# Optimization experiments

Hardware: AMD Instinct MI355X
Metric: run time of the kernel (lower is better)

Reference implementation:

```python
import jax, jax.numpy as jnp
import numpy as np
from jax import lax

D_MODEL = 1024
D_STATE = 16
D_CONV = 4
EXPAND = 2
HEADDIM = 64
D_INNER = EXPAND * D_MODEL            # 2048
NHEADS = D_INNER // HEADDIM           # 32
NGROUPS = 1
CONV_DIM = D_INNER + 2 * NGROUPS * D_STATE   # 2080
D_IN_PROJ = 2 * D_INNER + 2 * NGROUPS * D_STATE + NHEADS  # 4160
EPS = 1e-5


def _mamba2(x, in_proj_w, conv_w, conv_b, dt_bias, A_log, Dp, norm_w, out_proj_w):
    # x: (B, L, D_MODEL)
    Bt, L, _ = x.shape
    zxbcdt = jnp.einsum('bld,ed->ble', x, in_proj_w)  # (B,L,D_IN_PROJ)
    z, xBC, dt = jnp.split(zxbcdt, [D_INNER, D_INNER + CONV_DIM], axis=-1)
    dt = jax.nn.softplus(dt + dt_bias)               # (B,L,H)
    # depthwise causal conv over time
    xBC = jnp.swapaxes(xBC, 1, 2)                    # (B,C,L)
    xBC = lax.conv_general_dilated(
        xBC, conv_w, window_strides=(1,), padding=[(D_CONV - 1, 0)],
        feature_group_count=CONV_DIM,
        dimension_numbers=('NCH', 'OIH', 'NCH')) + conv_b[None, :, None]
    xBC = jnp.swapaxes(jax.nn.silu(xBC), 1, 2)       # (B,L,C)
    xs, Bm, Cm = jnp.split(xBC, [D_INNER, D_INNER + D_STATE], axis=-1)
    xs = xs.reshape(Bt, L, NHEADS, HEADDIM)          # (B,L,H,P)
    A = -jnp.exp(A_log)                              # (H,)
    dA = jnp.exp(dt * A)                             # (B,L,H)

    def step(h, inp):
        dA_t, dt_t, B_t, C_t, x_t = inp              # (B,H),(B,H),(B,N),(B,N),(B,H,P)
        h = h * dA_t[:, :, None, None] + jnp.einsum('bh,bn,bhp->bhpn', dt_t, B_t, x_t)
        y = jnp.einsum('bn,bhpn->bhp', C_t, h)
        return h, y

    h0 = jnp.zeros((Bt, NHEADS, HEADDIM, D_STATE), x.dtype)
    xs_seq = (jnp.swapaxes(dA, 0, 1), jnp.swapaxes(dt, 0, 1),
              jnp.swapaxes(Bm, 0, 1), jnp.swapaxes(Cm, 0, 1),
              jnp.swapaxes(xs, 0, 1))
    _, ys = lax.scan(step, h0, xs_seq)               # ys: (L,B,H,P)
    y = jnp.swapaxes(ys, 0, 1) + Dp[None, None, :, None] * xs
    y = y.reshape(Bt, L, D_INNER)
    # gated RMSNorm: gate first (norm_before_gate=False), then rmsnorm
    y = y * jax.nn.silu(z)
    y = y * lax.rsqrt(jnp.mean(y * y, axis=-1, keepdims=True) + EPS) * norm_w
    return jnp.einsum('bld,od->blo', y, out_proj_w)  # (B,L,D_MODEL)


def setup_inputs() -> dict:
    key = jax.random.key(0)
    ks = jax.random.split(key, 20)
    B, L = 2, 2048
    def mamba_params(kidx):
        k = jax.random.split(ks[kidx], 8)
        return dict(
            in_proj_w=jax.random.normal(k[0], (D_IN_PROJ, D_MODEL), jnp.float32) / np.sqrt(D_MODEL),
            conv_w=jax.random.normal(k[1], (CONV_DIM, 1, D_CONV), jnp.float32) / np.sqrt(D_CONV),
            conv_b=jax.random.normal(k[2], (CONV_DIM,), jnp.float32) * 0.01,
            dt_bias=jnp.log(jnp.expm1(jax.random.uniform(k[3], (NHEADS,), jnp.float32, 1e-3, 0.1))),
            A_log=jnp.log(jax.random.uniform(k[4], (NHEADS,), jnp.float32, 1.0, 16.0)),
            Dp=jnp.ones((NHEADS,), jnp.float32),
            norm_w=jnp.ones((D_INNER,), jnp.float32),
            out_proj_w=jax.random.normal(k[5], (D_MODEL, D_INNER), jnp.float32) / np.sqrt(D_INNER),
        )
    pf = mamba_params(1)
    pb = mamba_params(2)
    inp = {'x': jax.random.normal(ks[0], (B, L, D_MODEL), jnp.float32)}
    for name, p in (('fwd', pf), ('bwd', pb)):
        for pk, pv in p.items():
            inp[f'{name}_{pk}'] = pv
    inp['layer_out_proj_w'] = jax.random.normal(ks[3], (D_MODEL, 2 * D_MODEL), jnp.float32) / np.sqrt(2 * D_MODEL)
    inp['layer_scale'] = jnp.full((D_MODEL,), 1e-4, jnp.float32)
    return inp


def reference(x,
              fwd_in_proj_w, fwd_conv_w, fwd_conv_b, fwd_dt_bias, fwd_A_log, fwd_Dp, fwd_norm_w, fwd_out_proj_w,
              bwd_in_proj_w, bwd_conv_w, bwd_conv_b, bwd_dt_bias, bwd_A_log, bwd_Dp, bwd_norm_w, bwd_out_proj_w,
              layer_out_proj_w, layer_scale):
    h_fwd = _mamba2(x, fwd_in_proj_w, fwd_conv_w, fwd_conv_b, fwd_dt_bias, fwd_A_log, fwd_Dp, fwd_norm_w, fwd_out_proj_w)
    x_rev = jnp.flip(x, axis=1)
    h_bwd = jnp.flip(_mamba2(x_rev, bwd_in_proj_w, bwd_conv_w, bwd_conv_b, bwd_dt_bias, bwd_A_log, bwd_Dp, bwd_norm_w, bwd_out_proj_w), axis=1)
    h_bi = jnp.concatenate([h_fwd, h_bwd], axis=-1)   # (B,L,2*D_MODEL)
    mamba_out = jnp.einsum('ble,de->bld', h_bi, layer_out_proj_w)
    # dropout is identity in eval mode
    return x + mamba_out * layer_scale
```

## Files before the change

### kernel.cpp

```cpp
#include <hip/hip_runtime.h>

typedef __attribute__((ext_vector_type(8))) short bf16x8;
typedef __attribute__((ext_vector_type(4))) float f32x4;
typedef __attribute__((ext_vector_type(2))) long i64x2;

#define DEV static __device__ __forceinline__

DEV float b2f(unsigned short u) {
    union { unsigned int u; float f; } c; c.u = ((unsigned int)u) << 16; return c.f;
}
DEV unsigned short f2b(float f) {
    union { float f; unsigned int u; } c; c.f = f;
    unsigned int u = c.u + 0x7fffu + ((c.u >> 16) & 1u);
    return (unsigned short)(u >> 16);
}
DEV float silu_f(float v) { return v / (1.f + __expf(-v)); }

DEV unsigned short cvtpk2(float a, float b) {
    unsigned int d;
    asm("v_cvt_pk_fp8_f32 %0, %1, %2" : "=v"(d) : "v"(a), "v"(b));
    return (unsigned short)d;
}
DEV unsigned char cvt1(float a) { return (unsigned char)cvtpk2(a, 0.f); }

DEV int kperm(int gc) {
    return (gc & ~63) | (((gc >> 3) & 3) << 4) | (((gc >> 5) & 1) << 3) | (gc & 7);
}

#define GLD16(gp, lp) __builtin_amdgcn_global_load_lds( \
    (const __attribute__((address_space(1))) void*)(gp), \
    (__attribute__((address_space(3))) void*)(lp), 16, 0, 0)

#define LSEQ 2048
#define NB 2
#define RTOT 4096
#define DM 1024
#define DI 2048
#define NH 32
#define HP 64
#define NSTATE 16
#define CDIM 2080
#define DIP 4160
#define NW 8320
#define NWP 8448
#define QCH 64
#define NCH (LSEQ / QCH)

struct Cvt8Jobs {
    const float* s0[4];
    const float* s1[4];
    unsigned char* dst[4];
    int rows0[4], rows1[4], rowstot[4], shift[4];
};
__global__ __launch_bounds__(256) void cvt8b_kernel(Cvt8Jobs j) {
    const int jb = blockIdx.y;
    const int gid = blockIdx.x * 256 + threadIdx.x;
    const int shift = j.shift[jb];
    const int tpr = 1 << shift;
    if (gid >= (j.rowstot[jb] << shift)) return;
    const int row = gid >> shift, g = gid & (tpr - 1);
    const int blk = g >> 3, sub = g & 7, lq = sub >> 1, ks = sub & 1;
    const int K = tpr << 3;
    uint2 o;
    const int r0 = j.rows0[jb], r1 = j.rows1[jb];
    if (row < r0 + r1) {
        const float* src = (row < r0 ? j.s0[jb] + (size_t)row * K
                                     : j.s1[jb] + (size_t)(row - r0) * K)
                           + blk * 64 + ks * 32 + lq * 8;
        float4 v0 = *(const float4*)src;
        float4 v1 = *(const float4*)(src + 4);
        o.x = (unsigned)cvtpk2(v0.x, v0.y) | ((unsigned)cvtpk2(v0.z, v0.w) << 16);
        o.y = (unsigned)cvtpk2(v1.x, v1.y) | ((unsigned)cvtpk2(v1.z, v1.w) << 16);
    } else {
        o.x = 0; o.y = 0;
    }
    *(uint2*)(j.dst[jb] + (size_t)row * K + blk * 64 + sub * 8) = o;
}

template<int BM, int BN, int EPI>
__global__ void __launch_bounds__(512, 4)
gemm8_kernel(
    const unsigned char* __restrict__ A0, const unsigned char* __restrict__ B0,
    const unsigned char* __restrict__ A1, const unsigned char* __restrict__ B1,
    void* __restrict__ Cout,
    int Ntot, int K, int ldc, int coff0, int coff1,
    const float* __restrict__ ex, const float* __restrict__ esc)
{
    constexpr int NT = 512;
    constexpr int MF = BM / 32;
    constexpr int NI = BN / 64;
    constexpr int ABYTES = BM * 64;
    constexpr int BBYTES = BN * 64;
    constexpr int BUFB = ABYTES + BBYTES;
    constexpr int QA = ABYTES / (NT * 16);
    constexpr int QB = BBYTES / (NT * 16);
    constexpr int GT = QA + QB;
    __shared__ unsigned char lds8[4 * BUFB];

    const unsigned char* __restrict__ A8 = blockIdx.z ? A1 : A0;
    const unsigned char* __restrict__ B8 = blockIdx.z ? B1 : B0;
    const int coff = blockIdx.z ? coff1 : coff0;

    const int nbx = gridDim.x, nby = gridDim.y;
    const int nwg = nbx * nby;
    int id = blockIdx.y * nbx + blockIdx.x;
    {
        const int q = nwg >> 3, r = nwg & 7;
        const int xcd = id & 7, off = id >> 3;
        id = (xcd < r) ? (xcd * (q + 1) + off) : (r * (q + 1) + (xcd - r) * q + off);
    }
    const int gm = 8;
    const int gidx = id / (gm * nbx);
    const int rem  = id - gidx * gm * nbx;
    const int width = min(gm, nby - gidx * gm);
    const int bm = (gidx * gm + rem % width) * BM;
    const int bn = (rem / width) * BN;

    const int tid  = threadIdx.x;
    const int wave = tid >> 6, lane = tid & 63;
    const int wm = wave >> 2, wn = wave & 3;
    const int lr = lane & 15, lq = lane >> 4;
    const int KT = K >> 6;

    int aoff[MF], boff[NI];
#pragma unroll
    for (int mf = 0; mf < MF; ++mf) {
        int row = wm * (BM / 2) + mf * 16 + lr;
        int L = row >> 1, cc = ((row & 1) << 2) | lq;
        aoff[mf] = L * 128 + ((cc ^ (L & 7)) << 4);
    }
#pragma unroll
    for (int ni = 0; ni < NI; ++ni) {
        int row = wn * (BN / 4) + ni * 16 + lr;
        int L = row >> 1, cc = ((row & 1) << 2) | lq;
        boff[ni] = ABYTES + L * 128 + ((cc ^ (L & 7)) << 4);
    }

    auto stage = [&](int ktt, int sbuf) {
#pragma unroll
        for (int q = 0; q < QA; ++q) {
            int u = q * NT + tid;
            int L = u >> 3, cp = u & 7;
            int cc = cp ^ (L & 7);
            int srow = bm + 2 * L + (cc >> 2);
            const unsigned char* src = A8 + (size_t)srow * K + (ktt << 6) + ((cc & 3) << 4);
            GLD16(src, &lds8[sbuf * BUFB + q * (NT * 16) + (wave << 10)]);
        }
#pragma unroll
        for (int q = 0; q < QB; ++q) {
            int u = q * NT + tid;
            int L = u >> 3, cp = u & 7;
            int cc = cp ^ (L & 7);
            int srow = bn + 2 * L + (cc >> 2);
            const unsigned char* src = B8 + (size_t)srow * K + (ktt << 6) + ((cc & 3) << 4);
            GLD16(src, &lds8[sbuf * BUFB + ABYTES + q * (NT * 16) + (wave << 10)]);
        }
    };

    f32x4 acc[MF][NI];
#pragma unroll
    for (int i = 0; i < MF; ++i)
#pragma unroll
        for (int j = 0; j < NI; ++j) acc[i][j] = (f32x4){0.f, 0.f, 0.f, 0.f};

    stage(0, 0);
    if (KT > 1) stage(1, 1);
    if (KT > 2) stage(2, 2);
    if (KT > 2)      { asm volatile("s_waitcnt vmcnt(%0)" :: "n"(2 * GT) : "memory"); }
    else if (KT > 1) { asm volatile("s_waitcnt vmcnt(%0)" :: "n"(GT) : "memory"); }
    else             { asm volatile("s_waitcnt vmcnt(0)" ::: "memory"); }
    __builtin_amdgcn_sched_barrier(0);
    __builtin_amdgcn_s_barrier();
    __builtin_amdgcn_sched_barrier(0);

    for (int kt = 0; kt < KT; ++kt) {
        const int cb = (kt & 3) * BUFB;
        if (kt + 3 < KT) stage(kt + 3, (kt + 3) & 3);

        i64x2 av[MF], bv[NI];
#pragma unroll
        for (int mf = 0; mf < MF; ++mf) av[mf] = *(const i64x2*)&lds8[cb + aoff[mf]];
#pragma unroll
        for (int ni = 0; ni < NI; ++ni) bv[ni] = *(const i64x2*)&lds8[cb + boff[ni]];

        __builtin_amdgcn_s_setprio(1);
#pragma unroll
        for (int mf = 0; mf < MF; ++mf)
#pragma unroll
            for (int ni = 0; ni < NI; ++ni) {
                acc[mf][ni] = __builtin_amdgcn_mfma_f32_16x16x32_fp8_fp8(av[mf].x, bv[ni].x, acc[mf][ni], 0, 0, 0);
                acc[mf][ni] = __builtin_amdgcn_mfma_f32_16x16x32_fp8_fp8(av[mf].y, bv[ni].y, acc[mf][ni], 0, 0, 0);
            }
        __builtin_amdgcn_s_setprio(0);

        if (kt + 1 < KT) {
            if (kt + 3 < KT)      { asm volatile("s_waitcnt vmcnt(%0)" :: "n"(2 * GT) : "memory"); }
            else if (kt + 2 < KT) { asm volatile("s_waitcnt vmcnt(%0)" :: "n"(GT) : "memory"); }
            else                  { asm volatile("s_waitcnt vmcnt(0)" ::: "memory"); }
            __builtin_amdgcn_sched_barrier(0);
            __builtin_amdgcn_s_barrier();
            __builtin_amdgcn_sched_barrier(0);
        }
    }

#pragma unroll
    for (int mf = 0; mf < MF; ++mf)
#pragma unroll
        for (int ni = 0; ni < NI; ++ni)
#pragma unroll
            for (int r = 0; r < 4; ++r) {
                int grow = bm + wm * (BM / 2) + mf * 16 + lq * 4 + r;
                int gcol = bn + wn * (BN / 4) + ni * 16 + lr;
                float v = acc[mf][ni][r];
                if (EPI == 1) {
                    if (gcol < Ntot)
                        ((unsigned short*)Cout)[(size_t)grow * ldc + coff + gcol] = f2b(v);
                } else if (EPI == 2) {
                    size_t idx = (size_t)grow * ldc + gcol;
                    ((float*)Cout)[idx] = ex[idx] + v * esc[gcol];
                } else {
                    int gc = coff + gcol;
                    ((unsigned char*)Cout)[(size_t)grow * ldc + kperm(gc)] = cvt1(v);
                }
            }
}

#define TCV 32
__global__ __launch_bounds__(256) void conv_kernel(
    const unsigned short* __restrict__ ZX,
    const float* __restrict__ cwF, const float* __restrict__ cbF,
    const float* __restrict__ cwB, const float* __restrict__ cbB,
    const float* __restrict__ dtbiasF, const float* __restrict__ AlogF,
    const float* __restrict__ dtbiasB, const float* __restrict__ AlogB,
    unsigned short* __restrict__ xs,
    float* __restrict__ Bc, float* __restrict__ Cc,
    float* __restrict__ dtb, float* __restrict__ dAb)
{
    const int c = blockIdx.x * 256 + threadIdx.x;
    const int t0 = blockIdx.y * TCV;
    const int db = blockIdx.z;
    const int d = db >> 1, b = db & 1;

    if (c >= CDIM) {
        if (c >= CDIM + NH) return;
        const int h = c - CDIM;
        const float bias = (d ? dtbiasB : dtbiasF)[h];
        const float A = -__expf((d ? AlogB : AlogF)[h]);
        const unsigned short* zp = ZX + (size_t)d * DIP + (DI + CDIM) + h;
#pragma unroll 4
        for (int i = 0; i < TCV; ++i) {
            int t = t0 + i;
            float raw = b2f(zp[((size_t)b * LSEQ + t) * NW]);
            float xv = raw + bias;
            float dtv = (xv > 20.f) ? xv : __logf(1.f + __expf(xv));
            int idx = (db * LSEQ + t) * NH + h;
            dtb[idx] = dtv;
            dAb[idx] = __expf(dtv * A);
        }
        return;
    }

    const float* cw = d ? cwB : cwF;
    const float* cb = d ? cbB : cbF;
    float4 w = *(const float4*)&cw[c * 4];
    const float bias = cb[c];
    const unsigned short* base = ZX + (size_t)d * DIP + DI + c;

    auto ldg = [&](int t) -> float {
        return (t >= 0 && t < LSEQ) ? b2f(base[(size_t)(b * LSEQ + t) * NW]) : 0.f;
    };
    auto emit = [&](int t, float acc) {
        float v = silu_f(acc);
        const int row = b * LSEQ + t;
        if (c < DI) {
            xs[((size_t)d * RTOT + row) * DI + c] = f2b(v);
        } else if (c < DI + NSTATE) {
            Bc[((size_t)db * LSEQ + t) * NSTATE + (c - DI)] = v;
        } else {
            Cc[((size_t)db * LSEQ + t) * NSTATE + (c - DI - NSTATE)] = v;
        }
    };

    if (d == 0) {
        float v0 = ldg(t0 - 3), v1 = ldg(t0 - 2), v2 = ldg(t0 - 1), vt = ldg(t0);
#pragma unroll 4
        for (int i = 0; i < TCV; ++i) {
            float vn = (i < TCV - 1) ? ldg(t0 + i + 1) : 0.f;
            emit(t0 + i, bias + w.x * v0 + w.y * v1 + w.z * v2 + w.w * vt);
            v0 = v1; v1 = v2; v2 = vt; vt = vn;
        }
    } else {
        float v3 = ldg(t0 + TCV + 2), v2 = ldg(t0 + TCV + 1), v1 = ldg(t0 + TCV), vt = ldg(t0 + TCV - 1);
#pragma unroll 4
        for (int i = TCV - 1; i >= 0; --i) {
            float vn = (i > 0) ? ldg(t0 + i - 1) : 0.f;
            emit(t0 + i, bias + w.w * vt + w.z * v1 + w.y * v2 + w.x * v3);
            v3 = v2; v2 = v1; v1 = vt; vt = vn;
        }
    }
}

#define LD16V(dst, ptr) do { const float4* _p = (const float4*)(ptr); \
    float4 _q0 = _p[0], _q1 = _p[1], _q2 = _p[2], _q3 = _p[3]; \
    dst[0]=_q0.x; dst[1]=_q0.y; dst[2]=_q0.z; dst[3]=_q0.w; \
    dst[4]=_q1.x; dst[5]=_q1.y; dst[6]=_q1.z; dst[7]=_q1.w; \
    dst[8]=_q2.x; dst[9]=_q2.y; dst[10]=_q2.z; dst[11]=_q2.w; \
    dst[12]=_q3.x; dst[13]=_q3.y; dst[14]=_q3.z; dst[15]=_q3.w; } while (0)

#define ST16V(ptr, src) do { float4* _p = (float4*)(ptr); \
    _p[0] = make_float4(src[0],src[1],src[2],src[3]); \
    _p[1] = make_float4(src[4],src[5],src[6],src[7]); \
    _p[2] = make_float4(src[8],src[9],src[10],src[11]); \
    _p[3] = make_float4(src[12],src[13],src[14],src[15]); } while (0)

__global__ __launch_bounds__(64) void chunk_state_kernel(
    const unsigned short* __restrict__ xs,
    const float* __restrict__ Bc,
    const float* __restrict__ dtb, const float* __restrict__ dAb,
    float* __restrict__ Sbuf,
    float* __restrict__ Pbuf)
{
    const int h = blockIdx.x, db = blockIdx.y, c = blockIdx.z;
    const int d = db >> 1, b = db & 1;
    const int lane = threadIdx.x;
    float hs[16];
#pragma unroll
    for (int n = 0; n < 16; ++n) hs[n] = 0.f;
    float pacc = 1.f;
    const size_t dbase = (size_t)d * RTOT;
    const int s0 = c * QCH;

    float xq0, xq1, xq2, xq3, dtq0, dtq1, dtq2, dtq3, dAq0, dAq1, dAq2, dAq3;
    float BA[16], BB[16];

#define SIDX(ii) (d ? (LSEQ - 1 - (s0 + min((ii), QCH - 1))) : (s0 + min((ii), QCH - 1)))
#define XL(S, ii) do { const int _t = SIDX(ii); \
    const size_t _row = (size_t)b * LSEQ + _t, _rdb = (size_t)db * LSEQ + _t; \
    xq##S = b2f(xs[(dbase + _row) * DI + h * HP + lane]); \
    dtq##S = dtb[_rdb * 32 + h]; dAq##S = dAb[_rdb * 32 + h]; } while (0)
#define BL(BUF, ii) do { const int _t = SIDX(ii); \
    const size_t _rdb = (size_t)db * LSEQ + _t; LD16V(BUF, Bc + _rdb * 16); } while (0)
#define SC(S, BUF) do { const float _dtx = dtq##S * xq##S; \
    _Pragma("unroll") for (int n = 0; n < 16; ++n) hs[n] = fmaf(hs[n], dAq##S, BUF[n] * _dtx); \
    pacc *= dAq##S; } while (0)

    XL(0, 0); XL(1, 1); XL(2, 2);
    BL(BA, 0);
    for (int ii = 0; ii < QCH; ii += 4) {
        XL(3, ii + 3); BL(BB, ii + 1); SC(0, BA);
        XL(0, ii + 4); BL(BA, ii + 2); SC(1, BB);
        XL(1, ii + 5); BL(BB, ii + 3); SC(2, BA);
        XL(2, ii + 6); BL(BA, ii + 4); SC(3, BB);
    }
#undef SIDX
#undef XL
#undef BL
#undef SC

    float* Sp = Sbuf + (((size_t)(db * NH + h)) * NCH + c) * 1024 + lane * 16;
    ST16V(Sp, hs);
    if (lane == 0) Pbuf[(db * NH + h) * NCH + c] = pacc;
}

__global__ __launch_bounds__(64) void chunk_combine_kernel(
    const float* __restrict__ Sbuf, const float* __restrict__ Pbuf,
    float* __restrict__ Hbuf)
{
    const int idx = blockIdx.x;
    const int lane = threadIdx.x;
    float hs[16];
#pragma unroll
    for (int n = 0; n < 16; ++n) hs[n] = 0.f;
    float* H0 = Hbuf + ((size_t)idx * NCH) * 1024 + lane * 16;
    ST16V(H0, hs);
    for (int c = 0; c < NCH - 1; ++c) {
        const float* Sp = Sbuf + ((size_t)idx * NCH + c) * 1024 + lane * 16;
        float S[16];
        LD16V(S, Sp);
        const float P = Pbuf[idx * NCH + c];
#pragma unroll
        for (int n = 0; n < 16; ++n) hs[n] = fmaf(hs[n], P, S[n]);
        float* Hp = Hbuf + ((size_t)idx * NCH + c + 1) * 1024 + lane * 16;
        ST16V(Hp, hs);
    }
}

__global__ __launch_bounds__(64) void chunk_scan_kernel(
    const unsigned short* __restrict__ xs,
    const float* __restrict__ Bc, const float* __restrict__ Cc,
    const float* __restrict__ dtb, const float* __restrict__ dAb,
    const float* __restrict__ DpF, const float* __restrict__ DpB,
    const float* __restrict__ Hbuf,
    unsigned short* __restrict__ ybuf)
{
    const int h = blockIdx.x, db = blockIdx.y, c = blockIdx.z;
    const int d = db >> 1, b = db & 1;
    const int lane = threadIdx.x;
    const float Dp = (d ? DpB : DpF)[h];
    float hs[16];
    {
        const float* Hp = Hbuf + ((size_t)(db * NH + h) * NCH + c) * 1024 + lane * 16;
        LD16V(hs, Hp);
    }
    const size_t dbase = (size_t)d * RTOT;
    const int s0 = c * QCH;

    float xq0, xq1, xq2, xq3, dtq0, dtq1, dtq2, dtq3, dAq0, dAq1, dAq2, dAq3;
    float BA[16], BB[16], CA[16], CB[16];

#define SIDX(ii) (d ? (LSEQ - 1 - (s0 + min((ii), QCH - 1))) : (s0 + min((ii), QCH - 1)))
#define XL(S, ii) do { const int _t = SIDX(ii); \
    const size_t _row = (size_t)b * LSEQ + _t, _rdb = (size_t)db * LSEQ + _t; \
    xq##S = b2f(xs[(dbase + _row) * DI + h * HP + lane]); \
    dtq##S = dtb[_rdb * 32 + h]; dAq##S = dAb[_rdb * 32 + h]; } while (0)
#define BLC(BUF, CBUF, ii) do { const int _t = SIDX(ii); \
    const size_t _rdb = (size_t)db * LSEQ + _t; \
    LD16V(BUF, Bc + _rdb * 16); LD16V(CBUF, Cc + _rdb * 16); } while (0)
#define SCY(S, BUF, CBUF, iv) do { const float _dtx = dtq##S * xq##S; \
    float _y0 = 0.f, _y1 = 0.f, _y2 = 0.f, _y3 = 0.f; \
    _Pragma("unroll") for (int n = 0; n < 16; n += 4) { \
        hs[n]   = fmaf(hs[n],   dAq##S, BUF[n]   * _dtx); _y0 = fmaf(CBUF[n],   hs[n],   _y0); \
        hs[n+1] = fmaf(hs[n+1], dAq##S, BUF[n+1] * _dtx); _y1 = fmaf(CBUF[n+1], hs[n+1], _y1); \
        hs[n+2] = fmaf(hs[n+2], dAq##S, BUF[n+2] * _dtx); _y2 = fmaf(CBUF[n+2], hs[n+2], _y2); \
        hs[n+3] = fmaf(hs[n+3], dAq##S, BUF[n+3] * _dtx); _y3 = fmaf(CBUF[n+3], hs[n+3], _y3); } \
    const int _t = d ? (LSEQ - 1 - (s0 + (iv))) : (s0 + (iv)); \
    const size_t _row = (size_t)b * LSEQ + _t; \
    ybuf[(dbase + _row) * DI + h * HP + lane] = f2b(((_y0 + _y1) + (_y2 + _y3)) + Dp * xq##S); } while (0)

    XL(0, 0); XL(1, 1); XL(2, 2);
    BLC(BA, CA, 0);
    for (int ii = 0; ii < QCH; ii += 4) {
        XL(3, ii + 3); BLC(BB, CB, ii + 1); SCY(0, BA, CA, ii);
        XL(0, ii + 4); BLC(BA, CA, ii + 2); SCY(1, BB, CB, ii + 1);
        XL(1, ii + 5); BLC(BB, CB, ii + 3); SCY(2, BA, CA, ii + 2);
        XL(2, ii + 6); BLC(BA, CA, ii + 4); SCY(3, BB, CB, ii + 3);
    }
#undef SIDX
#undef XL
#undef BLC
#undef SCY
}

__global__ __launch_bounds__(256) void gatenorm_kernel(
    const unsigned short* __restrict__ ybuf, const unsigned short* __restrict__ ZX,
    const float* __restrict__ nwF, const float* __restrict__ nwB,
    unsigned char* __restrict__ yg8)
{
    const int r = blockIdx.x;
    const int d = blockIdx.y;
    const int tid = threadIdx.x;
    const float* nw = d ? nwB : nwF;
    const int c0 = tid * 8;
    const unsigned short* yp = ybuf + ((size_t)d * RTOT + r) * DI + c0;
    const unsigned short* zp = ZX + (size_t)r * NW + d * DIP + c0;
    uint4 yv = *(const uint4*)yp;
    uint4 zv = *(const uint4*)zp;
    unsigned int yw[4] = {yv.x, yv.y, yv.z, yv.w};
    unsigned int zw[4] = {zv.x, zv.y, zv.z, zv.w};
    float g[8]; float ss = 0.f;
#pragma unroll
    for (int i = 0; i < 8; ++i) {
        unsigned short yu = (i & 1) ? (unsigned short)(yw[i >> 1] >> 16) : (unsigned short)(yw[i >> 1] & 0xffff);
        unsigned short zu = (i & 1) ? (unsigned short)(zw[i >> 1] >> 16) : (unsigned short)(zw[i >> 1] & 0xffff);
        float y = b2f(yu), z = b2f(zu);
        float gv = y * silu_f(z);
        g[i] = gv; ss += gv * gv;
    }
#pragma unroll
    for (int m = 1; m < 64; m <<= 1) ss += __shfl_xor(ss, m, 64);
    __shared__ float red[4];
    if ((tid & 63) == 0) red[tid >> 6] = ss;
    __syncthreads();
    float tot = red[0] + red[1] + red[2] + red[3];
    float sc = rsqrtf(tot * (1.f / 2048.f) + 1e-5f);
    uint2 o;
    o.x = (unsigned)cvtpk2(g[0] * sc * nw[c0 + 0], g[1] * sc * nw[c0 + 1])
        | ((unsigned)cvtpk2(g[2] * sc * nw[c0 + 2], g[3] * sc * nw[c0 + 3]) << 16);
    o.y = (unsigned)cvtpk2(g[4] * sc * nw[c0 + 4], g[5] * sc * nw[c0 + 5])
        | ((unsigned)cvtpk2(g[6] * sc * nw[c0 + 6], g[7] * sc * nw[c0 + 7]) << 16);
    const int pos = (c0 & ~63) | (((c0 >> 3) & 3) << 4) | (((c0 >> 5) & 1) << 3);
    *(uint2*)(yg8 + ((size_t)d * RTOT + r) * DI + pos) = o;
}

extern "C" void kernel_launch(void* const* d_in, const int* in_sizes, int n_in,
                              void* d_out, int out_size, void* d_ws, size_t ws_size,
                              hipStream_t stream)
{
    const float* x     = (const float*)d_in[0];
    const float* fin   = (const float*)d_in[1];
    const float* fcw   = (const float*)d_in[2];
    const float* fcb   = (const float*)d_in[3];
    const float* fdtb  = (const float*)d_in[4];
    const float* fAlog = (const float*)d_in[5];
    const float* fDp   = (const float*)d_in[6];
    const float* fnw   = (const float*)d_in[7];
    const float* fout  = (const float*)d_in[8];
    const float* bin   = (const float*)d_in[9];
    const float* bcw   = (const float*)d_in[10];
    const float* bcb   = (const float*)d_in[11];
    const float* bdtb  = (const float*)d_in[12];
    const float* bAlog = (const float*)d_in[13];
    const float* bDp   = (const float*)d_in[14];
    const float* bnw   = (const float*)d_in[15];
    const float* bout  = (const float*)d_in[16];
    const float* lw    = (const float*)d_in[17];
    const float* lsc   = (const float*)d_in[18];

    char* w = (char*)d_ws;
    auto alloc = [&](size_t bytes) { char* p = w; w += (bytes + 255) & ~(size_t)255; return p; };
    unsigned char*  xb8  = (unsigned char*)alloc((size_t)RTOT * DM);
    unsigned char*  win8 = (unsigned char*)alloc((size_t)NWP * DM);
    unsigned char*  wo8  = (unsigned char*)alloc((size_t)2 * DM * DI);
    unsigned char*  wl8  = (unsigned char*)alloc((size_t)DM * DI);
    unsigned short* zx  = (unsigned short*)alloc((size_t)RTOT * NW * 2);
    unsigned short* xs  = (unsigned short*)alloc((size_t)2 * RTOT * DI * 2);
    float* Bc  = (float*)alloc((size_t)2 * RTOT * NSTATE * 4);
    float* Cc  = (float*)alloc((size_t)2 * RTOT * NSTATE * 4);
    float* dtb = (float*)alloc((size_t)2 * RTOT * NH * 4);
    float* dAb = (float*)alloc((size_t)2 * RTOT * NH * 4);
    unsigned short* yb  = (unsigned short*)alloc((size_t)2 * RTOT * DI * 2);
    unsigned char*  yg8 = (unsigned char*)alloc((size_t)2 * RTOT * DI);
    unsigned char*  hbi8= (unsigned char*)alloc((size_t)RTOT * DI);
    float* Pbuf = (float*)alloc((size_t)128 * NCH * 4);
    float* Sbuf = (float*)alloc((size_t)128 * NCH * 1024 * 4);
    float* Hbuf = (float*)alloc((size_t)128 * NCH * 1024 * 4);
    (void)ws_size; (void)in_sizes; (void)n_in; (void)out_size;

    Cvt8Jobs j;
    j.s0[0] = x;    j.s1[0] = x;    j.dst[0] = xb8;  j.rows0[0] = RTOT; j.rows1[0] = 0;    j.rowstot[0] = RTOT; j.shift[0] = 7;
    j.s0[1] = fin;  j.s1[1] = bin;  j.dst[1] = win8; j.rows0[1] = DIP;  j.rows1[1] = DIP;  j.rowstot[1] = NWP;  j.shift[1] = 7;
    j.s0[2] = fout; j.s1[2] = bout; j.dst[2] = wo8;  j.rows0[2] = DM;   j.rows1[2] = DM;   j.rowstot[2] = 2 * DM; j.shift[2] = 8;
    j.s0[3] = lw;   j.s1[3] = lw;   j.dst[3] = wl8;  j.rows0[3] = DM;   j.rows1[3] = 0;    j.rowstot[3] = DM;   j.shift[3] = 8;
    cvt8b_kernel<<<dim3((NWP * 128 + 255) / 256, 4), 256, 0, stream>>>(j);

    gemm8_kernel<128, 128, 1><<<dim3(NWP / 128, RTOT / 128), 512, 0, stream>>>(
        xb8, win8, nullptr, nullptr, zx, NW, DM, NW, 0, 0, nullptr, nullptr);

    conv_kernel<<<dim3((CDIM + NH + 255) / 256, LSEQ / TCV, 4), 256, 0, stream>>>(
        zx, fcw, fcb, bcw, bcb, fdtb, fAlog, bdtb, bAlog, xs, Bc, Cc, dtb, dAb);

    chunk_state_kernel<<<dim3(NH, 4, NCH - 1), 64, 0, stream>>>(
        xs, Bc, dtb, dAb, Sbuf, Pbuf);
    chunk_combine_kernel<<<128, 64, 0, stream>>>(Sbuf, Pbuf, Hbuf);
    chunk_scan_kernel<<<dim3(NH, 4, NCH), 64, 0, stream>>>(
        xs, Bc, Cc, dtb, dAb, fDp, bDp, Hbuf, yb);

    gatenorm_kernel<<<dim3(RTOT, 2), 256, 0, stream>>>(yb, zx, fnw, bnw, yg8);

    gemm8_kernel<128, 128, 3><<<dim3(DM / 128, RTOT / 128, 2), 512, 0, stream>>>(
        yg8, wo8, yg8 + (size_t)RTOT * DI, wo8 + (size_t)DM * DI,
        hbi8, DM, DI, DI, 0, DM, nullptr, nullptr);

    gemm8_kernel<128, 128, 2><<<dim3(DM / 128, RTOT / 128), 512, 0, stream>>>(
        hbi8, wl8, nullptr, nullptr, d_out, DM, DI, DM, 0, 0, x, lsc);
}
```

Baseline: 296.5 us.

## Add 256x256 FP8 in-projection GEMM with triple-buffered ping-pong pipeline

Replaces the 128x128 FP8 GEMM used for the input projection with a new 256x256-tile kernel. The new kernel uses a three-stage LDS ring with async global-to-LDS loads, XCD-aware block remapping with grouped tile ordering, and interleaves LDS reads, next-stage loads and MFMA quarters between barriers with raised wave priority. It aims for more data reuse per tile and better overlap of memory with compute. The cost is one workgroup per CU with 96KB LDS, fewer blocks in flight, and tile-divisibility assumptions on M and padded N.

Measured after the change: 319.6 us. +7.8%, slower.

```diff
diff --git a/kernel.cpp b/kernel.cpp
--- a/kernel.cpp
+++ b/kernel.cpp
@@ -77,6 +77,158 @@
     *(uint2*)(j.dst[jb] + (size_t)row * K + blk * 64 + sub * 8) = o;
 }
 
+#define PBARWAIT \
+    __builtin_amdgcn_s_barrier(); __builtin_amdgcn_sched_barrier(0); \
+    asm volatile("s_waitcnt lgkmcnt(0)" ::: "memory"); \
+    __builtin_amdgcn_sched_barrier(0);
+#define PENDBAR \
+    __builtin_amdgcn_s_barrier(); __builtin_amdgcn_sched_barrier(0);
+
+#define PLDA(AV, base0, MH) \
+    AV[0] = *(const i64x2*)&lds8[(base0) + aoff[(MH)*4 + 0]]; \
+    AV[1] = *(const i64x2*)&lds8[(base0) + aoff[(MH)*4 + 1]]; \
+    AV[2] = *(const i64x2*)&lds8[(base0) + aoff[(MH)*4 + 2]]; \
+    AV[3] = *(const i64x2*)&lds8[(base0) + aoff[(MH)*4 + 3]];
+#define PLDB(baseB, J0) \
+    bv[0] = *(const i64x2*)&lds8[(baseB) + boff[(J0)]]; \
+    bv[1] = *(const i64x2*)&lds8[(baseB) + boff[(J0) + 1]];
+#define PMM(AV, MH, NH) \
+    __builtin_amdgcn_s_setprio(1); \
+    _Pragma("unroll") \
+    for (int i = 0; i < 4; ++i) \
+    _Pragma("unroll") \
+        for (int jj = 0; jj < 2; ++jj) { \
+            acc[(MH)*4 + i][(NH)*2 + jj] = __builtin_amdgcn_mfma_f32_16x16x32_fp8_fp8(AV[i].x, bv[jj].x, acc[(MH)*4 + i][(NH)*2 + jj], 0, 0, 0); \
+            acc[(MH)*4 + i][(NH)*2 + jj] = __builtin_amdgcn_mfma_f32_16x16x32_fp8_fp8(AV[i].y, bv[jj].y, acc[(MH)*4 + i][(NH)*2 + jj], 0, 0, 0); \
+        } \
+    __builtin_amdgcn_s_setprio(0);
+
+__global__ void __launch_bounds__(512, 1)
+gemm8p_kernel(const unsigned char* __restrict__ A8, const unsigned char* __restrict__ B8,
+              unsigned short* __restrict__ Cout, int Ntot, int K, int ldc)
+{
+    __shared__ unsigned char lds8[98304];
+
+    const int nbx = gridDim.x, nby = gridDim.y;
+    const int nwg = nbx * nby;
+    int id = blockIdx.y * nbx + blockIdx.x;
+    {
+        const int q = nwg >> 3, r = nwg & 7;
+        const int xcd = id & 7, off = id >> 3;
+        id = (xcd < r) ? (xcd * (q + 1) + off) : (r * (q + 1) + (xcd - r) * q + off);
+    }
+    const int gm = 8;
+    const int gidx = id / (gm * nbx);
+    const int rem  = id - gidx * gm * nbx;
+    const int width = min(gm, nby - gidx * gm);
+    const int bm = (gidx * gm + rem % width) * 256;
+    const int bn = (rem / width) * 256;
+
+    const int tid  = threadIdx.x;
+    const int wave = tid >> 6, lane = tid & 63;
+    const int wm = wave >> 2, wn = wave & 3;
+    const int lr = lane & 15, lq = lane >> 4;
+    const int KT = K >> 6;
+
+    int aoff[8], boff[4];
+#pragma unroll
+    for (int mf = 0; mf < 8; ++mf) {
+        int row = wm * 128 + mf * 16 + lr;
+        int L = row >> 1, cc = ((row & 1) << 2) | lq;
+        aoff[mf] = L * 128 + ((cc ^ (L & 7)) << 4);
+    }
+#pragma unroll
+    for (int ni = 0; ni < 4; ++ni) {
+        int row = wn * 64 + ni * 16 + lr;
+        int L = row >> 1, cc = ((row & 1) << 2) | lq;
+        boff[ni] = L * 128 + ((cc ^ (L & 7)) << 4);
+    }
+
+    auto stgA = [&](int ktt, int q, int buf) {
+        int u = q * 512 + tid;
+        int L = u >> 3, cp = u & 7;
+        int cc = cp ^ (L & 7);
+        int srow = bm + 2 * L + (cc >> 2);
+        const unsigned char* src = A8 + (size_t)srow * K + (ktt << 6) + ((cc & 3) << 4);
+        GLD16(src, &lds8[buf * 16384 + q * 8192 + (wave << 10)]);
+    };
+    auto stgB = [&](int ktt, int q, int buf) {
+        int u = q * 512 + tid;
+        int L = u >> 3, cp = u & 7;
+        int cc = cp ^ (L & 7);
+        int srow = bn + 2 * L + (cc >> 2);
+        const unsigned char* src = B8 + (size_t)srow * K + (ktt << 6) + ((cc & 3) << 4);
+        GLD16(src, &lds8[49152 + buf * 16384 + q * 8192 + (wave << 10)]);
+    };
+
+    f32x4 acc[8][4];
+#pragma unroll
+    for (int i = 0; i < 8; ++i)
+#pragma unroll
+        for (int j = 0; j < 4; ++j) acc[i][j] = (f32x4){0.f, 0.f, 0.f, 0.f};
+
+    stgA(0, 0, 0); stgA(0, 1, 0); stgB(0, 0, 0); stgB(0, 1, 0);
+    if (KT > 1) { stgA(1, 0, 1); stgA(1, 1, 1); stgB(1, 0, 1); stgB(1, 1, 1); }
+    if (KT > 1) { asm volatile("s_waitcnt vmcnt(4)" ::: "memory"); }
+    else        { asm volatile("s_waitcnt vmcnt(0)" ::: "memory"); }
+    __builtin_amdgcn_sched_barrier(0);
+    __builtin_amdgcn_s_barrier();
+    __builtin_amdgcn_sched_barrier(0);
+
+    int cur = 0, sb = 2;
+    for (int kt = 0; kt < KT; ++kt) {
+        const int ca = cur * 16384;
+        const int cb = 49152 + cur * 16384;
+        const bool st = (kt + 2) < KT;
+        i64x2 avA[4], avB[4], bv[2];
+
+        PLDA(avA, ca, 0);
+        PLDB(cb, 0);
+        if (st) stgA(kt + 2, 0, sb);
+        PBARWAIT;
+        PMM(avA, 0, 0);
+        PENDBAR;
+
+        PLDA(avB, ca, 1);
+        if (st) stgA(kt + 2, 1, sb);
+        PBARWAIT;
+        PMM(avB, 1, 0);
+        PENDBAR;
+
+        PLDB(cb, 2);
+        if (st) stgB(kt + 2, 0, sb);
+        PBARWAIT;
+        PMM(avB, 1, 1);
+        PENDBAR;
+
+        if (st) stgB(kt + 2, 1, sb);
+        PBARWAIT;
+        PMM(avA, 0, 1);
+        if (kt + 1 < KT) {
+            if (st) { asm volatile("s_waitcnt vmcnt(4)" ::: "memory"); }
+            else    { asm volatile("s_waitcnt vmcnt(0)" ::: "memory"); }
+            __builtin_amdgcn_sched_barrier(0);
+            __builtin_amdgcn_s_barrier();
+            __builtin_amdgcn_sched_barrier(0);
+        }
+
+        cur = (cur == 2) ? 0 : cur + 1;
+        sb  = (sb == 2) ? 0 : sb + 1;
+    }
+
+#pragma unroll
+    for (int mf = 0; mf < 8; ++mf)
+#pragma unroll
+        for (int ni = 0; ni < 4; ++ni)
+#pragma unroll
+            for (int r = 0; r < 4; ++r) {
+                int grow = bm + wm * 128 + mf * 16 + lq * 4 + r;
+                int gcol = bn + wn * 64 + ni * 16 + lr;
+                if (gcol < Ntot)
+                    Cout[(size_t)grow * ldc + gcol] = f2b(acc[mf][ni][r]);
+            }
+}
+
 template<int BM, int BN, int EPI>
 __global__ void __launch_bounds__(512, 4)
 gemm8_kernel(
@@ -533,8 +685,8 @@
     j.s0[3] = lw;   j.s1[3] = lw;   j.dst[3] = wl8;  j.rows0[3] = DM;   j.rows1[3] = 0;    j.rowstot[3] = DM;   j.shift[3] = 8;
     cvt8b_kernel<<<dim3((NWP * 128 + 255) / 256, 4), 256, 0, stream>>>(j);
 
-    gemm8_kernel<128, 128, 1><<<dim3(NWP / 128, RTOT / 128), 512, 0, stream>>>(
-        xb8, win8, nullptr, nullptr, zx, NW, DM, NW, 0, 0, nullptr, nullptr);
+    gemm8p_kernel<<<dim3(NWP / 256, RTOT / 256), 512, 0, stream>>>(
+        xb8, win8, zx, NW, DM, NW);
 
     conv_kernel<<<dim3((CDIM + NH + 255) / 256, LSEQ / TCV, 4), 256, 0, stream>>>(
         zx, fcw, fcb, bcw, bcb, fdtb, fAlog, bdtb, bAlog, xs, Bc, Cc, dtb, dAb);
```
